# Optimization experiments

Hardware: AMD Instinct MI355X
Metric: run time of the kernel (lower is better)

The kernel has to match this reference:

```python
import jax, jax.numpy as jnp
import numpy as np

B, N, C = 16, 1024, 384
HEADS = 4
HIDDEN = 4 * C  # mlp_ratio=4 -> 1536
EPS = 1e-5


def layernorm(x, g, b):
    mu = jnp.mean(x, axis=-1, keepdims=True)
    var = jnp.mean((x - mu) ** 2, axis=-1, keepdims=True)
    return (x - mu) / jnp.sqrt(var + EPS) * g + b


def hardswish(x):
    return x * jnp.clip(x + 3.0, 0.0, 6.0) / 6.0


def setup_inputs() -> dict:
    key = jax.random.key(0)
    ks = jax.random.split(key, 8)
    s = 0.02
    return {
        "x": jax.random.normal(ks[0], (B, N, C), jnp.float32),
        "ln1_g": jnp.ones((C,), jnp.float32),
        "ln1_b": jnp.zeros((C,), jnp.float32),
        "Wqkv": jax.random.normal(ks[1], (3 * C, C), jnp.float32) * s,
        "Wproj": jax.random.normal(ks[2], (C, C), jnp.float32) * s,
        "bproj": jnp.zeros((C,), jnp.float32),
        "ln2_g": jnp.ones((C,), jnp.float32),
        "ln2_b": jnp.zeros((C,), jnp.float32),
        "Wfc1": jax.random.normal(ks[3], (HIDDEN, C, 1, 1), jnp.float32) * s,
        "bfc1": jnp.zeros((HIDDEN,), jnp.float32),
        "Wdw": jax.random.normal(ks[4], (HIDDEN, 1, 3, 3), jnp.float32) * s,
        "bdw": jnp.zeros((HIDDEN,), jnp.float32),
        "Wfc2": jax.random.normal(ks[5], (C, HIDDEN, 1, 1), jnp.float32) * s,
        "bfc2": jnp.zeros((C,), jnp.float32),
        "H": 32,
        "W": 32,
    }


def reference(x, ln1_g, ln1_b, Wqkv, Wproj, bproj, ln2_g, ln2_b,
              Wfc1, bfc1, Wdw, bdw, Wfc2, bfc2, H, W):
    b, n, c = x.shape
    h = HEADS
    hd = c // h
    # --- attention branch ---
    xn = layernorm(x, ln1_g, ln1_b)
    qkv = xn @ Wqkv.T  # [B,N,3C]
    qkv = qkv.reshape(b, n, h, 3, hd).transpose(3, 0, 2, 1, 4)  # [3,B,h,N,hd]
    q, k, v = qkv[0], qkv[1], qkv[2]
    attn = jax.nn.softmax(jnp.einsum('bhnd,bhmd->bhnm', q, k) * (hd ** -0.5), axis=-1)
    o = jnp.einsum('bhnm,bhmd->bhnd', attn, v)  # [B,h,N,hd]
    o = o.transpose(0, 2, 1, 3).reshape(b, n, c)
    o = o @ Wproj.T + bproj
    x = x + o
    # --- IRB (inverted residual conv MLP) branch ---
    y = layernorm(x, ln2_g, ln2_b)
    y = y.transpose(0, 2, 1).reshape(b, c, H, W)  # NCHW
    dn = ('NCHW', 'OIHW', 'NCHW')
    y = jax.lax.conv_general_dilated(y, Wfc1, (1, 1), 'VALID', dimension_numbers=dn)
    y = hardswish(y + bfc1[None, :, None, None])
    y = jax.lax.conv_general_dilated(y, Wdw, (1, 1), 'SAME',
                                     feature_group_count=Wdw.shape[0],
                                     dimension_numbers=dn)
    y = hardswish(y + bdw[None, :, None, None])
    y = jax.lax.conv_general_dilated(y, Wfc2, (1, 1), 'VALID', dimension_numbers=dn)
    y = y + bfc2[None, :, None, None]
    y = y.reshape(b, c, n).transpose(0, 2, 1)
    return x + y
```

## Files before the change

kernel.cpp:

```cpp
#include <hip/hip_runtime.h>
#include <hip/hip_bf16.h>
#include <math.h>

#define BB 16
#define NN 1024
#define CC 384
#define HEADS 4
#define HD 96
#define HID 1536
#define MROWS (BB*NN)

typedef __attribute__((ext_vector_type(8))) short bf16x8;
typedef __attribute__((ext_vector_type(8))) ushort u16x8;
typedef __attribute__((ext_vector_type(4))) float f32x4;

__device__ __forceinline__ float hswish(float x) {
    float t = fminf(fmaxf(x + 3.0f, 0.0f), 6.0f);
    return x * t * (1.0f / 6.0f);
}

__device__ __forceinline__ ushort f2bf(float f) {
    union { float f; unsigned u; } v; v.f = f;
    unsigned r = v.u + 0x7fff + ((v.u >> 16) & 1);
    return (ushort)(r >> 16);
}

__device__ __forceinline__ float bf2f(ushort u) {
    union { unsigned u; float f; } v; v.u = ((unsigned)u) << 16;
    return v.f;
}

__device__ __forceinline__ void gload16(const ushort* g, ushort* l) {
    __builtin_amdgcn_global_load_lds(
        (const __attribute__((address_space(1))) void*)g,
        (__attribute__((address_space(3))) void*)l, 16, 0, 0);
}

#define S_QKV (1152*384)
#define S_P   (384*384)
#define S_1   (1536*384)
#define S_2   (384*1536)
#define S_ALL (S_QKV + S_P + S_1 + S_2)
#define WBLKS (S_ALL / (256 * 8))

__device__ __forceinline__ void ln_body(
    const float* __restrict__ x, const float* __restrict__ g,
    const float* __restrict__ b, ushort* __restrict__ y, int row)
{
    int lane = threadIdx.x & 63;
    const float* xr = x + (size_t)row * CC;
    float v[6];
    float s = 0.f;
#pragma unroll
    for (int j = 0; j < 6; ++j) { v[j] = xr[lane + 64 * j]; s += v[j]; }
#pragma unroll
    for (int off = 32; off; off >>= 1) s += __shfl_xor(s, off, 64);
    float mu = s * (1.0f / CC);
    float s2 = 0.f;
#pragma unroll
    for (int j = 0; j < 6; ++j) { float d = v[j] - mu; s2 += d * d; }
#pragma unroll
    for (int off = 32; off; off >>= 1) s2 += __shfl_xor(s2, off, 64);
    float rinv = rsqrtf(s2 * (1.0f / CC) + 1e-5f);
    ushort* yr = y + (size_t)row * CC;
#pragma unroll
    for (int j = 0; j < 6; ++j) {
        int c = lane + 64 * j;
        yr[c] = f2bf((v[j] - mu) * rinv * g[c] + b[c]);
    }
}

__global__ __launch_bounds__(256) void prep(
    const float* __restrict__ wqkv, const float* __restrict__ wproj,
    const float* __restrict__ wfc1, const float* __restrict__ wfc2,
    ushort* __restrict__ dq, ushort* __restrict__ dp,
    ushort* __restrict__ d1, ushort* __restrict__ d2,
    const float* __restrict__ x, const float* __restrict__ g1,
    const float* __restrict__ b1, ushort* __restrict__ y)
{
    int blk = blockIdx.x;
    if (blk >= WBLKS) {
        int row = (blk - WBLKS) * 4 + (threadIdx.x >> 6);
        ln_body(x, g1, b1, y, row);
        return;
    }
    int i = (blk * 256 + threadIdx.x) * 8;
    const float* src;
    ushort* dst;
    int off, scaled = 0;
    if (i < S_QKV) {
        src = wqkv; dst = dq; off = i;
        scaled = ((off / 384) % 288) < 96;
    } else if (i < S_QKV + S_P) {
        src = wproj; dst = dp; off = i - S_QKV;
    } else if (i < S_QKV + S_P + S_1) {
        src = wfc1; dst = d1; off = i - S_QKV - S_P;
    } else {
        src = wfc2; dst = d2; off = i - S_QKV - S_P - S_1;
    }
    float4 a = *(const float4*)(src + off);
    float4 c = *(const float4*)(src + off + 4);
    float sc = scaled ? 0.10206207261596577f : 1.0f;
    u16x8 o;
    o[0] = f2bf(a.x * sc); o[1] = f2bf(a.y * sc);
    o[2] = f2bf(a.z * sc); o[3] = f2bf(a.w * sc);
    o[4] = f2bf(c.x * sc); o[5] = f2bf(c.y * sc);
    o[6] = f2bf(c.z * sc); o[7] = f2bf(c.w * sc);
    *(u16x8*)(dst + off) = o;
}

__global__ __launch_bounds__(256) void ln_kernel(
    const float* __restrict__ x, const float* __restrict__ g,
    const float* __restrict__ b, ushort* __restrict__ y)
{
    int row = blockIdx.x * 4 + (threadIdx.x >> 6);
    ln_body(x, g, b, y, row);
}

template<int BN>
__global__ __launch_bounds__(256) void gemm_mfma(
    const ushort* __restrict__ A, const ushort* __restrict__ B,
    const float* __restrict__ bias, const float* __restrict__ res,
    float* __restrict__ Cf, ushort* __restrict__ Cb,
    int M, int N, int K, int act)
{
    constexpr int NF = BN / 32;
    __shared__ ushort As[128][64];
    __shared__ ushort Bs[BN][64];
    int tid = threadIdx.x;
    int lane = tid & 63, w = tid >> 6;
    int wr = w >> 1, wc = w & 1;
    int g = lane >> 4, li = lane & 15;

    int nx = N / BN;
    int bid = blockIdx.x;
    int rr = bid & 7, qq = bid >> 3;
    int xx = qq % nx, yy = (qq / nx) * 8 + rr;
    int m0 = yy * 128, n0 = xx * BN;

    int srow = tid >> 3;
    int scol = ((tid & 7) ^ (srow & 7)) * 8;

    f32x4 acc[4][NF];
#pragma unroll
    for (int m = 0; m < 4; ++m)
#pragma unroll
        for (int n = 0; n < NF; ++n) acc[m][n] = (f32x4){0.f, 0.f, 0.f, 0.f};

    for (int k0 = 0; k0 < K; k0 += 64) {
        __syncthreads();
#pragma unroll
        for (int j = 0; j < 4; ++j)
            gload16(A + (size_t)(m0 + j * 32 + srow) * K + k0 + scol,
                    &As[j * 32 + w * 8][0]);
#pragma unroll
        for (int j = 0; j < BN / 32; ++j)
            gload16(B + (size_t)(n0 + j * 32 + srow) * K + k0 + scol,
                    &Bs[j * 32 + w * 8][0]);
        __syncthreads();
#pragma unroll
        for (int s = 0; s < 2; ++s) {
            bf16x8 af[4], bfr[NF];
#pragma unroll
            for (int m = 0; m < 4; ++m) {
                int row = wr * 64 + m * 16 + li;
                af[m] = *(const bf16x8*)&As[row][((s * 4 + g) ^ (row & 7)) * 8];
            }
#pragma unroll
            for (int n = 0; n < NF; ++n) {
                int row = wc * (BN / 2) + n * 16 + li;
                bfr[n] = *(const bf16x8*)&Bs[row][((s * 4 + g) ^ (row & 7)) * 8];
            }
            __builtin_amdgcn_s_setprio(1);
#pragma unroll
            for (int m = 0; m < 4; ++m)
#pragma unroll
                for (int n = 0; n < NF; ++n)
                    acc[m][n] = __builtin_amdgcn_mfma_f32_16x16x32_bf16(
                        af[m], bfr[n], acc[m][n], 0, 0, 0);
            __builtin_amdgcn_s_setprio(0);
        }
    }

#pragma unroll
    for (int m = 0; m < 4; ++m)
#pragma unroll
        for (int n = 0; n < NF; ++n) {
            int col = n0 + wc * (BN / 2) + n * 16 + li;
            float bv = bias ? bias[col] : 0.f;
#pragma unroll
            for (int r = 0; r < 4; ++r) {
                int row = m0 + wr * 64 + m * 16 + g * 4 + r;
                float v = acc[m][n][r] + bv;
                if (act == 1) v = hswish(v);
                if (res) v += res[(size_t)row * N + col];
                if (Cb) Cb[(size_t)row * N + col] = f2bf(v);
                else    Cf[(size_t)row * N + col] = v;
            }
        }
}

__global__ __launch_bounds__(256) void gemm_qkv(
    const ushort* __restrict__ A, const ushort* __restrict__ B,
    ushort* __restrict__ Qb, ushort* __restrict__ Kb, ushort* __restrict__ Vt,
    int M)
{
    constexpr int K = CC;
    __shared__ ushort sh[128 * 64 * 2];
    ushort* As = sh;
    ushort* Bs = sh + 128 * 64;
    ushort* VtS = sh;
    int tid = threadIdx.x;
    int lane = tid & 63, w = tid >> 6;
    int wr = w >> 1, wc = w & 1;
    int g = lane >> 4, li = lane & 15;

    const int nx = 9;
    int bid = blockIdx.x;
    int rr = bid & 7, qq = bid >> 3;
    int xx = qq % nx, yy = (qq / nx) * 8 + rr;
    int m0 = yy * 128, n0 = xx * 128;

    int srow = tid >> 3;
    int scol = ((tid & 7) ^ (srow & 7)) * 8;

    f32x4 acc[4][4];
#pragma unroll
    for (int m = 0; m < 4; ++m)
#pragma unroll
        for (int n = 0; n < 4; ++n) acc[m][n] = (f32x4){0.f, 0.f, 0.f, 0.f};

    for (int k0 = 0; k0 < K; k0 += 64) {
        __syncthreads();
#pragma unroll
        for (int j = 0; j < 4; ++j) {
            gload16(A + (size_t)(m0 + j * 32 + srow) * K + k0 + scol,
                    &As[(j * 32 + w * 8) * 64]);
            gload16(B + (size_t)(n0 + j * 32 + srow) * K + k0 + scol,
                    &Bs[(j * 32 + w * 8) * 64]);
        }
        __syncthreads();
#pragma unroll
        for (int s = 0; s < 2; ++s) {
            bf16x8 af[4], bfr[4];
#pragma unroll
            for (int m = 0; m < 4; ++m) {
                int row = wr * 64 + m * 16 + li;
                af[m] = *(const bf16x8*)&As[row * 64 + ((s * 4 + g) ^ (row & 7)) * 8];
            }
#pragma unroll
            for (int n = 0; n < 4; ++n) {
                int row = wc * 64 + n * 16 + li;
                bfr[n] = *(const bf16x8*)&Bs[row * 64 + ((s * 4 + g) ^ (row & 7)) * 8];
            }
            __builtin_amdgcn_s_setprio(1);
#pragma unroll
            for (int m = 0; m < 4; ++m)
#pragma unroll
                for (int n = 0; n < 4; ++n)
                    acc[m][n] = __builtin_amdgcn_mfma_f32_16x16x32_bf16(
                        af[m], bfr[n], acc[m][n], 0, 0, 0);
            __builtin_amdgcn_s_setprio(0);
        }
    }

    int d0 = 0, d1 = 0, hv = 0;
#pragma unroll
    for (int hh = 0; hh < 4; ++hh) {
        int vlo = 192 + 288 * hh, vhi = 288 + 288 * hh;
        int lo = n0 > vlo ? n0 : vlo;
        int hi = (n0 + 128) < vhi ? (n0 + 128) : vhi;
        if (hi > lo) { hv = hh; d0 = lo - vlo; d1 = hi - vlo; }
    }
    int b0 = m0 >> 10, ntok0 = m0 & 1023;

    __syncthreads();

#pragma unroll
    for (int m = 0; m < 4; ++m)
#pragma unroll
        for (int n = 0; n < 4; ++n) {
            int col = n0 + wc * 64 + n * 16 + li;
            int h = col / 288;
            int rem = col - h * 288;
            int which = rem / 96;
            int d = rem - which * 96;
#pragma unroll
            for (int r = 0; r < 4; ++r) {
                int row = wr * 64 + m * 16 + g * 4 + r;
                ushort bv = f2bf(acc[m][n][r]);
                if (which == 2) {
                    VtS[(d - d0) * 136 + row] = bv;
                } else {
                    int tok = m0 + row;
                    int bq = tok >> 10, ntok = tok & 1023;
                    int bh = bq * HEADS + h;
                    (which ? Kb : Qb)[((size_t)bh * NN + ntok) * HD + d] = bv;
                }
            }
        }
    __syncthreads();

    int dspan = d1 - d0;
    int bhv = b0 * HEADS + hv;
    for (int idx = tid; idx < dspan * 16; idx += 256) {
        int dd = idx >> 4, u0 = (idx & 15) * 8;
        bf16x8 val = *(const bf16x8*)&VtS[dd * 136 + u0];
        *(bf16x8*)(Vt + ((size_t)bhv * HD + d0 + dd) * NN + ntok0 + u0) = val;
    }
}

#define KSTR 128
#define VSTR 64
#define PPAD 72

__global__ __launch_bounds__(256) void attn_mfma(
    const ushort* __restrict__ Qb, const ushort* __restrict__ Kb,
    const ushort* __restrict__ Vt, ushort* __restrict__ o)
{
    __shared__ ushort Klds[64 * KSTR];
    __shared__ ushort Vlds[96 * VSTR];
    __shared__ ushort Plds[4][16][PPAD];
    int tid = threadIdx.x;
    int lane = tid & 63, w = tid >> 6;
    int g = lane >> 4, li = lane & 15;
    int bid = blockIdx.x;
    int qt = bid >> 6, bh = bid & 63;
    int q0 = qt * 64;
    int b = bh >> 2, h = bh & 3;

    bf16x8 vones;
#pragma unroll
    for (int e = 0; e < 8; ++e) vones[e] = (short)0x3F80;

    const ushort* qrow = Qb + ((size_t)bh * NN + q0 + w * 16 + li) * HD;
    bf16x8 qf[3];
#pragma unroll
    for (int s = 0; s < 3; ++s)
        qf[s] = *(const bf16x8*)(qrow + s * 32 + g * 8);

    f32x4 oacc[7];
#pragma unroll
    for (int dt = 0; dt < 7; ++dt) oacc[dt] = (f32x4){0.f, 0.f, 0.f, 0.f};

    const size_t kbase = (size_t)bh * NN;
    const size_t vbase = (size_t)bh * HD;

    for (int t = 0; t < NN / 64; ++t) {
        int n0 = t * 64;
        __syncthreads();
#pragma unroll
        for (int j = 0; j < 4; ++j) {
            int row = w * 16 + j * 4 + (lane >> 4);
            gload16(Kb + (kbase + n0 + row) * HD + (((lane & 15) ^ (row & 7)) << 3),
                    &Klds[(w * 16 + j * 4) * KSTR]);
        }
#pragma unroll
        for (int j = 0; j < 3; ++j) {
            int row = w * 24 + j * 8 + (lane >> 3);
            gload16(Vt + (vbase + row) * NN + n0 + (((lane & 7) ^ (row & 7)) << 3),
                    &Vlds[(w * 24 + j * 8) * VSTR]);
        }
        __syncthreads();

        f32x4 sacc[4];
#pragma unroll
        for (int c = 0; c < 4; ++c) sacc[c] = (f32x4){0.f, 0.f, 0.f, 0.f};
        __builtin_amdgcn_s_setprio(1);
#pragma unroll
        for (int s = 0; s < 3; ++s)
#pragma unroll
            for (int c = 0; c < 4; ++c) {
                bf16x8 kf = *(const bf16x8*)&Klds[(c * 16 + li) * KSTR +
                                                  (((s * 4 + g) ^ (li & 7)) << 3)];
                sacc[c] = __builtin_amdgcn_mfma_f32_16x16x32_bf16(qf[s], kf, sacc[c], 0, 0, 0);
            }
        __builtin_amdgcn_s_setprio(0);

#pragma unroll
        for (int r = 0; r < 4; ++r)
#pragma unroll
            for (int c = 0; c < 4; ++c)
                Plds[w][g * 4 + r][c * 16 + li] = f2bf(__expf(sacc[c][r]));

        __builtin_amdgcn_s_setprio(1);
#pragma unroll
        for (int sub = 0; sub < 2; ++sub) {
            bf16x8 pf = *(const bf16x8*)&Plds[w][li][sub * 32 + g * 8];
#pragma unroll
            for (int dt = 0; dt < 6; ++dt) {
                bf16x8 vf = *(const bf16x8*)&Vlds[(dt * 16 + li) * VSTR +
                                                  (((sub * 4 + g) ^ (li & 7)) << 3)];
                oacc[dt] = __builtin_amdgcn_mfma_f32_16x16x32_bf16(pf, vf, oacc[dt], 0, 0, 0);
            }
            oacc[6] = __builtin_amdgcn_mfma_f32_16x16x32_bf16(pf, vones, oacc[6], 0, 0, 0);
        }
        __builtin_amdgcn_s_setprio(0);
    }

    float inv[4];
#pragma unroll
    for (int r = 0; r < 4; ++r) inv[r] = 1.0f / oacc[6][r];
#pragma unroll
    for (int dt = 0; dt < 6; ++dt)
#pragma unroll
        for (int r = 0; r < 4; ++r) {
            int row = q0 + w * 16 + g * 4 + r;
            int col = h * HD + dt * 16 + li;
            o[(size_t)(b * NN + row) * CC + col] = f2bf(oacc[dt][r] * inv[r]);
        }
}

__global__ __launch_bounds__(256) void dw_kernel(
    const ushort* __restrict__ h1, const float* __restrict__ w,
    const float* __restrict__ bias, ushort* __restrict__ h2)
{
    int tid = threadIdx.x;
    int c0 = blockIdx.x * 256 + (tid & 63) * 4;
    int x = blockIdx.y * 4 + (tid >> 6);
    int b = blockIdx.z;
    const ushort* base = h1 + (size_t)b * NN * HID + c0;
    ushort* obase = h2 + (size_t)b * NN * HID + c0;

    float wv[4][9];
#pragma unroll
    for (int q = 0; q < 4; ++q)
#pragma unroll
        for (int k = 0; k < 9; ++k) wv[q][k] = w[(c0 + q) * 9 + k];
    float bv[4];
#pragma unroll
    for (int q = 0; q < 4; ++q) bv[q] = bias[c0 + q];

    bool xm = (x > 0), xp = (x < 31);

    float win[2][3][4];
#pragma unroll
    for (int a = 0; a < 2; ++a)
#pragma unroll
        for (int p = 0; p < 3; ++p)
#pragma unroll
            for (int q = 0; q < 4; ++q) win[a][p][q] = 0.f;

    {
        const ushort* rp = base + (size_t)x * HID;
        if (xm) { ushort4 u = *(const ushort4*)(rp - HID);
            win[1][0][0]=bf2f(u.x); win[1][0][1]=bf2f(u.y); win[1][0][2]=bf2f(u.z); win[1][0][3]=bf2f(u.w); }
        { ushort4 u = *(const ushort4*)rp;
            win[1][1][0]=bf2f(u.x); win[1][1][1]=bf2f(u.y); win[1][1][2]=bf2f(u.z); win[1][1][3]=bf2f(u.w); }
        if (xp) { ushort4 u = *(const ushort4*)(rp + HID);
            win[1][2][0]=bf2f(u.x); win[1][2][1]=bf2f(u.y); win[1][2][2]=bf2f(u.z); win[1][2][3]=bf2f(u.w); }
    }

#pragma unroll
    for (int y = 0; y < 32; ++y) {
        float nw[3][4];
#pragma unroll
        for (int p = 0; p < 3; ++p)
#pragma unroll
            for (int q = 0; q < 4; ++q) nw[p][q] = 0.f;
        if (y < 31) {
            const ushort* rp = base + (size_t)((y + 1) * 32 + x) * HID;
            if (xm) { ushort4 u = *(const ushort4*)(rp - HID);
                nw[0][0]=bf2f(u.x); nw[0][1]=bf2f(u.y); nw[0][2]=bf2f(u.z); nw[0][3]=bf2f(u.w); }
            { ushort4 u = *(const ushort4*)rp;
                nw[1][0]=bf2f(u.x); nw[1][1]=bf2f(u.y); nw[1][2]=bf2f(u.z); nw[1][3]=bf2f(u.w); }
            if (xp) { ushort4 u = *(const ushort4*)(rp + HID);
                nw[2][0]=bf2f(u.x); nw[2][1]=bf2f(u.y); nw[2][2]=bf2f(u.z); nw[2][3]=bf2f(u.w); }
        }
        ushort4 ov;
        ushort* po = (ushort*)&ov;
#pragma unroll
        for (int q = 0; q < 4; ++q) {
            float a = bv[q];
            a = fmaf(win[0][0][q], wv[q][0], a);
            a = fmaf(win[0][1][q], wv[q][1], a);
            a = fmaf(win[0][2][q], wv[q][2], a);
            a = fmaf(win[1][0][q], wv[q][3], a);
            a = fmaf(win[1][1][q], wv[q][4], a);
            a = fmaf(win[1][2][q], wv[q][5], a);
            a = fmaf(nw[0][q], wv[q][6], a);
            a = fmaf(nw[1][q], wv[q][7], a);
            a = fmaf(nw[2][q], wv[q][8], a);
            po[q] = f2bf(hswish(a));
        }
        *(ushort4*)&obase[(size_t)(y * 32 + x) * HID] = ov;
#pragma unroll
        for (int p = 0; p < 3; ++p)
#pragma unroll
            for (int q = 0; q < 4; ++q) {
                win[0][p][q] = win[1][p][q];
                win[1][p][q] = nw[p][q];
            }
    }
}

extern "C" void kernel_launch(void* const* d_in, const int* in_sizes, int n_in,
                              void* d_out, int out_size, void* d_ws, size_t ws_size,
                              hipStream_t stream) {
    const float* x     = (const float*)d_in[0];
    const float* ln1_g = (const float*)d_in[1];
    const float* ln1_b = (const float*)d_in[2];
    const float* Wqkv  = (const float*)d_in[3];
    const float* Wproj = (const float*)d_in[4];
    const float* bproj = (const float*)d_in[5];
    const float* ln2_g = (const float*)d_in[6];
    const float* ln2_b = (const float*)d_in[7];
    const float* Wfc1  = (const float*)d_in[8];
    const float* bfc1  = (const float*)d_in[9];
    const float* Wdw   = (const float*)d_in[10];
    const float* bdw   = (const float*)d_in[11];
    const float* Wfc2  = (const float*)d_in[12];
    const float* bfc2  = (const float*)d_in[13];
    float* out = (float*)d_out;

    const int M = MROWS;
    ushort* abuf = (ushort*)d_ws;
    ushort* Qb   = abuf + (size_t)M * 384;
    ushort* Kb   = Qb   + (size_t)M * 384;
    ushort* Vt   = Kb   + (size_t)M * 384;
    ushort* obuf = Vt   + (size_t)M * 384;
    ushort* h1   = obuf + (size_t)M * 384;
    ushort* h2   = h1   + (size_t)M * 1536;
    ushort* wq   = h2   + (size_t)M * 1536;
    ushort* wp   = wq   + 1152 * 384;
    ushort* w1   = wp   + 384 * 384;
    ushort* w2   = w1   + 1536 * 384;

    prep<<<WBLKS + M / 4, 256, 0, stream>>>(
        Wqkv, Wproj, Wfc1, Wfc2, wq, wp, w1, w2, x, ln1_g, ln1_b, abuf);
    gemm_qkv<<<9 * (M / 128), 256, 0, stream>>>(abuf, wq, Qb, Kb, Vt, M);
    attn_mfma<<<1024, 256, 0, stream>>>(Qb, Kb, Vt, obuf);
    gemm_mfma<64><<<(CC / 64) * (M / 128), 256, 0, stream>>>(
        obuf, wp, bproj, x, out, nullptr, M, CC, CC, 0);
    ln_kernel<<<M / 4, 256, 0, stream>>>(out, ln2_g, ln2_b, abuf);
    gemm_mfma<64><<<(HID / 64) * (M / 128), 256, 0, stream>>>(
        abuf, w1, bfc1, nullptr, nullptr, h1, M, HID, CC, 1);
    dw_kernel<<<dim3(HID / 256, 8, BB), 256, 0, stream>>>(h1, Wdw, bdw, h2);
    gemm_mfma<64><<<(CC / 64) * (M / 128), 256, 0, stream>>>(
        h2, w2, bfc2, out, out, nullptr, M, CC, HID, 0);
}
```

Measured before the change: 228.1 us.

## Add 256x64-tile GEMM for fc1 and fold log2e into Q scale for exp2

Adds a new bf16 MFMA GEMM kernel with 256-row by 64-column tiles, where each wave computes a 64x64 sub-tile, and uses it for the fc1 projection with fused bias and hardswish. This halves the number of blocks and raises A-tile reuse per B load. Separately, the Q weight scale now includes log2(e), so attention can call exp2f instead of __expf and save a multiply per score. The larger tile uses more LDS and registers per block and launches fewer blocks, which may lower occupancy.

```diff
diff --git a/kernel.cpp b/kernel.cpp
--- a/kernel.cpp
+++ b/kernel.cpp
@@ -100,7 +100,7 @@
     }
     float4 a = *(const float4*)(src + off);
     float4 c = *(const float4*)(src + off + 4);
-    float sc = scaled ? 0.10206207261596577f : 1.0f;
+    float sc = scaled ? 0.14724615088646412f : 1.0f;
     u16x8 o;
     o[0] = f2bf(a.x * sc); o[1] = f2bf(a.y * sc);
     o[2] = f2bf(a.z * sc); o[3] = f2bf(a.w * sc);
@@ -196,6 +196,83 @@
                 if (res) v += res[(size_t)row * N + col];
                 if (Cb) Cb[(size_t)row * N + col] = f2bf(v);
                 else    Cf[(size_t)row * N + col] = v;
+            }
+        }
+}
+
+__global__ __launch_bounds__(256) void gemm_mfma256(
+    const ushort* __restrict__ A, const ushort* __restrict__ B,
+    const float* __restrict__ bias, ushort* __restrict__ Cb,
+    int M, int N, int K, int act)
+{
+    __shared__ ushort As[256][64];
+    __shared__ ushort Bs[64][64];
+    int tid = threadIdx.x;
+    int lane = tid & 63, w = tid >> 6;
+    int g = lane >> 4, li = lane & 15;
+
+    int nx = N / 64;
+    int bid = blockIdx.x;
+    int rr = bid & 7, qq = bid >> 3;
+    int xx = qq % nx, yy = (qq / nx) * 8 + rr;
+    int m0 = yy * 256, n0 = xx * 64;
+
+    int srow = tid >> 3;
+    int scol = ((tid & 7) ^ (srow & 7)) * 8;
+
+    f32x4 acc[4][4];
+#pragma unroll
+    for (int m = 0; m < 4; ++m)
+#pragma unroll
+        for (int n = 0; n < 4; ++n) acc[m][n] = (f32x4){0.f, 0.f, 0.f, 0.f};
+
+    for (int k0 = 0; k0 < K; k0 += 64) {
+        __syncthreads();
+#pragma unroll
+        for (int j = 0; j < 8; ++j)
+            gload16(A + (size_t)(m0 + j * 32 + srow) * K + k0 + scol,
+                    &As[j * 32 + w * 8][0]);
+#pragma unroll
+        for (int j = 0; j < 2; ++j)
+            gload16(B + (size_t)(n0 + j * 32 + srow) * K + k0 + scol,
+                    &Bs[j * 32 + w * 8][0]);
+        __syncthreads();
+#pragma unroll
+        for (int s = 0; s < 2; ++s) {
+            bf16x8 af[4], bfr[4];
+#pragma unroll
+            for (int m = 0; m < 4; ++m) {
+                int row = w * 64 + m * 16 + li;
+                af[m] = *(const bf16x8*)&As[row][((s * 4 + g) ^ (row & 7)) * 8];
+            }
+#pragma unroll
+            for (int n = 0; n < 4; ++n) {
+                int row = n * 16 + li;
+                bfr[n] = *(const bf16x8*)&Bs[row][((s * 4 + g) ^ (row & 7)) * 8];
+            }
+            __builtin_amdgcn_s_setprio(1);
+#pragma unroll
+            for (int m = 0; m < 4; ++m)
+#pragma unroll
+                for (int n = 0; n < 4; ++n)
+                    acc[m][n] = __builtin_amdgcn_mfma_f32_16x16x32_bf16(
+                        af[m], bfr[n], acc[m][n], 0, 0, 0);
+            __builtin_amdgcn_s_setprio(0);
+        }
+    }
+
+#pragma unroll
+    for (int m = 0; m < 4; ++m)
+#pragma unroll
+        for (int n = 0; n < 4; ++n) {
+            int col = n0 + n * 16 + li;
+            float bv = bias ? bias[col] : 0.f;
+#pragma unroll
+            for (int r = 0; r < 4; ++r) {
+                int row = m0 + w * 64 + m * 16 + g * 4 + r;
+                float v = acc[m][n][r] + bv;
+                if (act == 1) v = hswish(v);
+                Cb[(size_t)row * N + col] = f2bf(v);
             }
         }
 }
@@ -381,7 +458,7 @@
         for (int r = 0; r < 4; ++r)
 #pragma unroll
             for (int c = 0; c < 4; ++c)
-                Plds[w][g * 4 + r][c * 16 + li] = f2bf(__expf(sacc[c][r]));
+                Plds[w][g * 4 + r][c * 16 + li] = f2bf(exp2f(sacc[c][r]));
 
         __builtin_amdgcn_s_setprio(1);
 #pragma unroll
@@ -533,8 +610,8 @@
     gemm_mfma<64><<<(CC / 64) * (M / 128), 256, 0, stream>>>(
         obuf, wp, bproj, x, out, nullptr, M, CC, CC, 0);
     ln_kernel<<<M / 4, 256, 0, stream>>>(out, ln2_g, ln2_b, abuf);
-    gemm_mfma<64><<<(HID / 64) * (M / 128), 256, 0, stream>>>(
-        abuf, w1, bfc1, nullptr, nullptr, h1, M, HID, CC, 1);
+    gemm_mfma256<<<(HID / 64) * (M / 256), 256, 0, stream>>>(
+        abuf, w1, bfc1, h1, M, HID, CC, 1);
     dw_kernel<<<dim3(HID / 256, 8, BB), 256, 0, stream>>>(h1, Wdw, bdw, h2);
     gemm_mfma<64><<<(CC / 64) * (M / 128), 256, 0, stream>>>(
         h2, w2, bfc2, out, out, nullptr, M, CC, HID, 0);
```

Measured after the change: 231.2 us. About the same (+1.4%).
